# Optimization experiments

Measured on AMD Instinct MI355X. Metric: run time of the kernel, lower is better.

The kernel has to match this reference:

```python
import jax, jax.numpy as jnp
import numpy as np

H = 128
N_CAN = 100000
N_FLAG = 50000
E = 600000
L = 500000


def _sage_conv(x_src, x_dst, edge_index, Wl, bl, Wr):
    # PyG SAGEConv (mean aggr): lin_l(mean_{j in N(i)} x_j) + lin_r(x_i)
    src, dst = edge_index[0], edge_index[1]
    msg = x_src[src]                                        # [E, H] gather
    n_dst = x_dst.shape[0]
    agg = jax.ops.segment_sum(msg, dst, num_segments=n_dst)  # [N_dst, H]
    cnt = jax.ops.segment_sum(jnp.ones((msg.shape[0],), msg.dtype), dst,
                              num_segments=n_dst)
    mean = agg / jnp.maximum(cnt, 1.0)[:, None]
    return mean @ Wl.T + bl + x_dst @ Wr.T


def setup_inputs() -> dict:
    key = jax.random.key(0)
    ks = jax.random.split(key, 16)
    s = 1.0 / np.sqrt(H)
    inp = {
        'can_node_id': jnp.arange(N_CAN, dtype=jnp.int64) if jax.config.jax_enable_x64 else jnp.arange(N_CAN, dtype=jnp.int32),
        'flag_node_id': jnp.arange(N_FLAG, dtype=jnp.int32),
        'edge_index_cf': jnp.stack([
            jax.random.randint(ks[0], (E,), 0, N_CAN),
            jax.random.randint(ks[1], (E,), 0, N_FLAG)]),
        'edge_index_fc': jnp.stack([
            jax.random.randint(ks[2], (E,), 0, N_FLAG),
            jax.random.randint(ks[3], (E,), 0, N_CAN)]),
        'edge_label_index': jnp.stack([
            jax.random.randint(ks[4], (L,), 0, N_CAN),
            jax.random.randint(ks[5], (L,), 0, N_FLAG)]),
        'can_emb': jax.random.normal(ks[6], (N_CAN, H), jnp.float32),
        'flag_emb': jax.random.normal(ks[7], (N_FLAG, H), jnp.float32),
        # SAGEConv for edge type CAN->flag (updates flag nodes)
        'Wl_cf': jax.random.normal(ks[8], (H, H), jnp.float32) * s,
        'bl_cf': jnp.zeros((H,), jnp.float32),
        'Wr_cf': jax.random.normal(ks[9], (H, H), jnp.float32) * s,
        # SAGEConv for edge type flag->CAN (updates CAN nodes)
        'Wl_fc': jax.random.normal(ks[10], (H, H), jnp.float32) * s,
        'bl_fc': jnp.zeros((H,), jnp.float32),
        'Wr_fc': jax.random.normal(ks[11], (H, H), jnp.float32) * s,
        # classifier MLP
        'W1': jax.random.normal(ks[12], (H, 2 * H), jnp.float32) * (1.0 / np.sqrt(2 * H)),
        'b1': jnp.zeros((H,), jnp.float32),
        'W2': jax.random.normal(ks[13], (1, H), jnp.float32) * s,
        'b2': jnp.zeros((1,), jnp.float32),
    }
    return inp


def reference(can_node_id, flag_node_id, edge_index_cf, edge_index_fc,
              edge_label_index, can_emb, flag_emb,
              Wl_cf, bl_cf, Wr_cf, Wl_fc, bl_fc, Wr_fc,
              W1, b1, W2, b2):
    # embedding lookups
    x_can = can_emb[can_node_id]    # [N_CAN, H]
    x_flag = flag_emb[flag_node_id]  # [N_FLAG, H]
    # to_hetero single SAGE layer + relu (dropout is identity in eval)
    upd_flag = jax.nn.relu(_sage_conv(x_can, x_flag, edge_index_cf, Wl_cf, bl_cf, Wr_cf))
    upd_can = jax.nn.relu(_sage_conv(x_flag, x_can, edge_index_fc, Wl_fc, bl_fc, Wr_fc))
    # link prediction classifier
    src = upd_can[edge_label_index[0]]   # [L, H]
    dst = upd_flag[edge_label_index[1]]  # [L, H]
    h = jax.nn.relu(jnp.concatenate([src, dst], axis=-1) @ W1.T + b1)
    out = h @ W2.T + b2
    return out.reshape(-1)
```

## Files before the change

### kernel.cpp

```cpp
#include <hip/hip_runtime.h>
#include <hip/hip_bf16.h>

#define H 128
#define BSH 8
#define MAXB 1024

typedef __attribute__((ext_vector_type(8))) short short8;
typedef __attribute__((ext_vector_type(4))) short short4v;
typedef __attribute__((ext_vector_type(4))) float floatx4;
typedef unsigned short ushort_t;
typedef unsigned int uint_t;

__device__ __forceinline__ short f2bf(float f) {
    __hip_bfloat16 h = __float2bfloat16(f);
    return *reinterpret_cast<short*>(&h);
}
__device__ __forceinline__ float bflo(uint_t u) { return __uint_as_float(u << 16); }
__device__ __forceinline__ float bfhi(uint_t u) { return __uint_as_float(u & 0xFFFF0000u); }
__device__ __forceinline__ uint_t pack_bf2(float x, float y) {
    return (uint_t)(ushort_t)f2bf(x) | ((uint_t)(ushort_t)f2bf(y) << 16);
}

__global__ __launch_bounds__(256)
void bucket_hist_cvt_kernel(const int* __restrict__ ei1, const int* __restrict__ ei2,
                            int E, int NF, int B, int* __restrict__ bcnt, int nbh,
                            const float* __restrict__ a, int n4a,
                            const float* __restrict__ b, int n4b,
                            ushort_t* __restrict__ da, ushort_t* __restrict__ db,
                            const float* __restrict__ Wl_cf, const float* __restrict__ Wr_cf,
                            const float* __restrict__ Wl_fc, const float* __restrict__ Wr_fc,
                            const float* __restrict__ W1, ushort_t* __restrict__ wb) {
    __shared__ int h[MAXB];
    int tid = threadIdx.x;
    if ((int)blockIdx.x < nbh) {
        for (int i = tid; i < B; i += 256) h[i] = 0;
        __syncthreads();
        int base = blockIdx.x * 4096;
        #pragma unroll 4
        for (int it = 0; it < 16; ++it) {
            int t = base + it * 256 + tid;
            if (t < 2 * E) {
                int g = (t < E) ? ei1[E + t] : (ei2[E + t - E] + NF);
                atomicAdd(&h[g >> BSH], 1);
            }
        }
        __syncthreads();
        for (int i = tid; i < B; i += 256)
            if (h[i]) atomicAdd(&bcnt[i], h[i]);
        return;
    }
    int i = ((int)blockIdx.x - nbh) * 256 + tid;
    const float* src; ushort_t* dst; int k;
    if (i < n4a) { src = a; dst = da; k = i; }
    else if (i < n4a + n4b) { src = b; dst = db; k = i - n4a; }
    else {
        int idx = (i - n4a - n4b) * 4;
        if (idx >= 98304) return;
        int off;
        if      (idx < 16384) { src = Wl_cf; off = idx; }
        else if (idx < 32768) { src = Wr_cf; off = idx - 16384; }
        else if (idx < 49152) { src = Wl_fc; off = idx - 32768; }
        else if (idx < 65536) { src = Wr_fc; off = idx - 49152; }
        else                  { src = W1;    off = idx - 65536; }
        float4 v = *(const float4*)(src + off);
        short4v s;
        s[0] = f2bf(v.x); s[1] = f2bf(v.y); s[2] = f2bf(v.z); s[3] = f2bf(v.w);
        *(short4v*)(wb + idx) = s;
        return;
    }
    float4 v = ((const float4*)src)[k];
    short4v s;
    s[0] = f2bf(v.x); s[1] = f2bf(v.y); s[2] = f2bf(v.z); s[3] = f2bf(v.w);
    ((short4v*)dst)[k] = s;
}

__global__ __launch_bounds__(256)
void partition_kernel(const int* __restrict__ ei1, const int* __restrict__ ei2,
                      int E, int NF, int B, const int* __restrict__ bcnt,
                      int* __restrict__ bfront, uint_t* __restrict__ part) {
    __shared__ int h[MAXB];
    __shared__ int basex[MAXB];
    __shared__ int sdata[256];
    int tid = threadIdx.x;
    {
        int base4 = tid * 4;
        int v[4]; int s = 0;
        #pragma unroll
        for (int i = 0; i < 4; ++i) { int idx = base4 + i; v[i] = (idx < B) ? bcnt[idx] : 0; s += v[i]; }
        sdata[tid] = s;
        __syncthreads();
        for (int off = 1; off < 256; off <<= 1) {
            int t = (tid >= off) ? sdata[tid - off] : 0;
            __syncthreads();
            sdata[tid] += t;
            __syncthreads();
        }
        int excl = tid ? sdata[tid - 1] : 0;
        #pragma unroll
        for (int i = 0; i < 4; ++i) {
            int idx = base4 + i;
            if (idx < B) basex[idx] = excl;
            excl += v[i];
        }
    }
    for (int i = tid; i < B; i += 256) h[i] = 0;
    __syncthreads();
    int base = blockIdx.x * 4096;
    #pragma unroll 4
    for (int it = 0; it < 16; ++it) {
        int t = base + it * 256 + tid;
        if (t < 2 * E) {
            int g = (t < E) ? ei1[E + t] : (ei2[E + t - E] + NF);
            atomicAdd(&h[g >> BSH], 1);
        }
    }
    __syncthreads();
    for (int i = tid; i < B; i += 256) {
        int c = h[i];
        if (c) basex[i] += atomicAdd(&bfront[i], c);
    }
    __syncthreads();
    for (int i = tid; i < B; i += 256) h[i] = 0;
    __syncthreads();
    #pragma unroll 4
    for (int it = 0; it < 16; ++it) {
        int t = base + it * 256 + tid;
        if (t < 2 * E) {
            int g, s;
            if (t < E) { g = ei1[E + t]; s = ei1[t]; }
            else       { int e = t - E; g = ei2[E + e] + NF; s = ei2[e]; }
            int bk = g >> BSH;
            int r = atomicAdd(&h[bk], 1);
            part[basex[bk] + r] = ((uint_t)(g & 255) << 24) | (uint_t)s;
        }
    }
}

__global__ __launch_bounds__(256)
void fine_bin_kernel(const int* __restrict__ bcnt, int B, int nTot, int E2,
                     const uint_t* __restrict__ part,
                     int* __restrict__ offs, int* __restrict__ bins) {
    __shared__ int cnt[256];
    __shared__ int sdata[256];
    __shared__ int excl[256];
    int b = blockIdx.x;
    int tid = threadIdx.x;
    {
        int partial = 0;
        for (int i = tid; i < b; i += 256) partial += bcnt[i];
        sdata[tid] = partial;
        __syncthreads();
        for (int off = 128; off > 0; off >>= 1) {
            if (tid < off) sdata[tid] += sdata[tid + off];
            __syncthreads();
        }
    }
    int seg0 = sdata[0];
    int seg1 = seg0 + bcnt[b];
    int gbase = b << BSH;
    __syncthreads();
    cnt[tid] = 0;
    __syncthreads();
    for (int k = seg0 + tid; k < seg1; k += 256)
        atomicAdd(&cnt[part[k] >> 24], 1);
    __syncthreads();
    sdata[tid] = cnt[tid];
    __syncthreads();
    for (int off = 1; off < 256; off <<= 1) {
        int t = (tid >= off) ? sdata[tid - off] : 0;
        __syncthreads();
        sdata[tid] += t;
        __syncthreads();
    }
    excl[tid] = tid ? sdata[tid - 1] : 0;
    int g = gbase + tid;
    if (g < nTot) offs[g] = seg0 + excl[tid];
    if (b == 0 && tid == 0) offs[nTot] = E2;
    cnt[tid] = 0;
    __syncthreads();
    for (int k = seg0 + tid; k < seg1; k += 256) {
        uint_t e = part[k];
        int l = (int)(e >> 24);
        int r = atomicAdd(&cnt[l], 1);
        bins[seg0 + excl[l] + r] = (int)(e & 0x00FFFFFFu);
    }
}

__global__ __launch_bounds__(256)
void gather_mean3_kernel(const int* __restrict__ offs, int nTotal, int split,
                         const int* __restrict__ bins,
                         const ushort_t* __restrict__ embA, ushort_t* __restrict__ aggA,
                         const ushort_t* __restrict__ embB, ushort_t* __restrict__ aggB) {
    int g = blockIdx.x * 4 + (threadIdx.x >> 6);
    if (g >= nTotal) return;
    int lane = threadIdx.x & 63;
    int q = lane >> 4, l15 = lane & 15;
    int start = offs[g];
    int end = offs[g + 1];
    int deg = end - start;
    const ushort_t* emb; ushort_t* agg; int row;
    if (g < split) { emb = embA; agg = aggA; row = g; }
    else           { emb = embB; agg = aggB; row = g - split; }

    float acc[8];
    #pragma unroll
    for (int t = 0; t < 8; ++t) acc[t] = 0.f;

    int nPre = deg < 64 ? deg : 64;
    int pre = (lane < nPre) ? bins[start + lane] : 0;

    int col = l15 * 8;
    for (int it = 0; it < (nPre + 7) / 8; ++it) {
        int e0 = 8 * it + q;
        int e1 = e0 + 4;
        int s0 = __shfl(pre, e0, 64);
        int s1 = __shfl(pre, e1, 64);
        if (e0 < nPre) {
            uint4 r = *(const uint4*)(emb + (size_t)s0 * H + col);
            acc[0] += bflo(r.x); acc[1] += bfhi(r.x);
            acc[2] += bflo(r.y); acc[3] += bfhi(r.y);
            acc[4] += bflo(r.z); acc[5] += bfhi(r.z);
            acc[6] += bflo(r.w); acc[7] += bfhi(r.w);
        }
        if (e1 < nPre) {
            uint4 r = *(const uint4*)(emb + (size_t)s1 * H + col);
            acc[0] += bflo(r.x); acc[1] += bfhi(r.x);
            acc[2] += bflo(r.y); acc[3] += bfhi(r.y);
            acc[4] += bflo(r.z); acc[5] += bfhi(r.z);
            acc[6] += bflo(r.w); acc[7] += bfhi(r.w);
        }
    }
    for (int k = start + 64 + q; k < end; k += 4) {
        int s = bins[k];
        uint4 r = *(const uint4*)(emb + (size_t)s * H + col);
        acc[0] += bflo(r.x); acc[1] += bfhi(r.x);
        acc[2] += bflo(r.y); acc[3] += bfhi(r.y);
        acc[4] += bflo(r.z); acc[5] += bfhi(r.z);
        acc[6] += bflo(r.w); acc[7] += bfhi(r.w);
    }

    #pragma unroll
    for (int t = 0; t < 8; ++t) {
        acc[t] += __shfl_xor(acc[t], 16, 64);
        acc[t] += __shfl_xor(acc[t], 32, 64);
    }
    if (q == 0) {
        float inv = 1.0f / fmaxf((float)deg, 1.0f);
        uint4 o;
        o.x = pack_bf2(acc[0] * inv, acc[1] * inv);
        o.y = pack_bf2(acc[2] * inv, acc[3] * inv);
        o.z = pack_bf2(acc[4] * inv, acc[5] * inv);
        o.w = pack_bf2(acc[6] * inv, acc[7] * inv);
        *(uint4*)(agg + (size_t)row * H + col) = o;
    }
}

__global__ __launch_bounds__(256)
void sage2_kernel(int nbF, int NF, int NC,
                  ushort_t* __restrict__ aggf, const ushort_t* __restrict__ embf,
                  ushort_t* __restrict__ aggc, const ushort_t* __restrict__ embc,
                  const ushort_t* __restrict__ wlf, const ushort_t* __restrict__ wrf,
                  const float* __restrict__ blf,
                  const ushort_t* __restrict__ wlc, const ushort_t* __restrict__ wrc,
                  const float* __restrict__ blc,
                  const ushort_t* __restrict__ W1) {
    __shared__ short A[64][264];
    bool isF = (int)blockIdx.x < nbF;
    int nrows = isF ? NF : NC;
    int rbase = (isF ? blockIdx.x : blockIdx.x - nbF) * 64;
    ushort_t* io = isF ? aggf : aggc;
    const ushort_t* emb = isF ? embf : embc;
    const ushort_t* Wl = isF ? wlf : wlc;
    const ushort_t* Wr = isF ? wrf : wrc;
    const float* bl = isF ? blf : blc;
    int koff = isF ? 128 : 0;

    int tid = threadIdx.x;
    int lane = tid & 63;
    int wv = tid >> 6;
    int l15 = lane & 15;
    int quad = lane >> 4;
    int nb0 = 32 * wv + l15;

    for (int idx = tid; idx < 64 * 64; idx += 256) {
        int r = idx >> 6, qq = idx & 63;
        int row = rbase + r;
        short4v s = (short4v){0, 0, 0, 0};
        if (row < nrows) {
            const ushort_t* src = (qq < 32) ? (io + (size_t)row * H + qq * 4)
                                            : (emb + (size_t)row * H + (qq - 32) * 4);
            s = *(const short4v*)src;
        }
        *(short4v*)&A[r][qq * 4] = s;
    }

    floatx4 acc[4][2];
    #pragma unroll
    for (int i = 0; i < 4; ++i)
        #pragma unroll
        for (int j = 0; j < 2; ++j)
            acc[i][j] = (floatx4){0.f, 0.f, 0.f, 0.f};

    float blv0 = bl[nb0];
    float blv1 = bl[nb0 + 16];
    __syncthreads();

    #pragma unroll
    for (int half = 0; half < 2; ++half) {
        const ushort_t* W = half ? Wr : Wl;
        #pragma unroll
        for (int ks = 0; ks < 4; ++ks) {
            int kb = ks * 32 + quad * 8;
            short8 b0 = *(const short8*)(W + (size_t)nb0 * H + kb);
            short8 b1 = *(const short8*)(W + (size_t)(nb0 + 16) * H + kb);
            int ka = half * 128 + kb;
            #pragma unroll
            for (int mt = 0; mt < 4; ++mt) {
                short8 a = *(const short8*)&A[16 * mt + l15][ka];
                acc[mt][0] = __builtin_amdgcn_mfma_f32_16x16x32_bf16(a, b0, acc[mt][0], 0, 0, 0);
                acc[mt][1] = __builtin_amdgcn_mfma_f32_16x16x32_bf16(a, b1, acc[mt][1], 0, 0, 0);
            }
        }
    }

    __syncthreads();
    #pragma unroll
    for (int mt = 0; mt < 4; ++mt)
        #pragma unroll
        for (int nt = 0; nt < 2; ++nt) {
            float blv = nt ? blv1 : blv0;
            int colw = nb0 + 16 * nt;
            #pragma unroll
            for (int rg = 0; rg < 4; ++rg) {
                int row = 16 * mt + quad * 4 + rg;
                A[row][colw] = f2bf(fmaxf(acc[mt][nt][rg] + blv, 0.0f));
                acc[mt][nt][rg] = 0.0f;
            }
        }
    __syncthreads();

    const ushort_t* W1p = W1 + koff;
    #pragma unroll
    for (int ks = 0; ks < 4; ++ks) {
        int kb = ks * 32 + quad * 8;
        short8 b0 = *(const short8*)(W1p + (size_t)nb0 * 256 + kb);
        short8 b1 = *(const short8*)(W1p + (size_t)(nb0 + 16) * 256 + kb);
        #pragma unroll
        for (int mt = 0; mt < 4; ++mt) {
            short8 a = *(const short8*)&A[16 * mt + l15][kb];
            acc[mt][0] = __builtin_amdgcn_mfma_f32_16x16x32_bf16(a, b0, acc[mt][0], 0, 0, 0);
            acc[mt][1] = __builtin_amdgcn_mfma_f32_16x16x32_bf16(a, b1, acc[mt][1], 0, 0, 0);
        }
    }

    #pragma unroll
    for (int mt = 0; mt < 4; ++mt)
        #pragma unroll
        for (int rg = 0; rg < 4; ++rg) {
            int row = rbase + 16 * mt + quad * 4 + rg;
            if (row < nrows) {
                io[(size_t)row * H + nb0]      = (ushort_t)f2bf(acc[mt][0][rg]);
                io[(size_t)row * H + nb0 + 16] = (ushort_t)f2bf(acc[mt][1][rg]);
            }
        }
}

__global__ __launch_bounds__(256)
void hist2_kernel(const int* __restrict__ ei1, const int* __restrict__ ei2, int E,
                  int* __restrict__ deg1, int* __restrict__ deg2) {
    int t = blockIdx.x * 256 + threadIdx.x;
    if (t < E) atomicAdd(&deg1[ei1[E + t]], 1);
    else if (t < 2 * E) { int e = t - E; atomicAdd(&deg2[ei2[E + e]], 1); }
}

__global__ __launch_bounds__(256)
void scan_blocksum_kernel(const int* __restrict__ deg, int n, int* __restrict__ bsums) {
    __shared__ int sdata[256];
    int tid = threadIdx.x;
    int base = blockIdx.x * 1024 + tid * 4;
    int v = 0;
    #pragma unroll
    for (int i = 0; i < 4; ++i) { int idx = base + i; if (idx < n) v += deg[idx]; }
    sdata[tid] = v;
    __syncthreads();
    for (int off = 128; off > 0; off >>= 1) {
        if (tid < off) sdata[tid] += sdata[tid + off];
        __syncthreads();
    }
    if (tid == 0) bsums[blockIdx.x] = sdata[0];
}

__global__ __launch_bounds__(256)
void scan_write_kernel(int* __restrict__ data, int n, const int* __restrict__ bsums) {
    __shared__ int sdata[256];
    __shared__ int boff;
    int tid = threadIdx.x;
    if (tid < 64) {
        int acc = 0;
        for (int i = tid; i < (int)blockIdx.x; i += 64) acc += bsums[i];
        #pragma unroll
        for (int off = 32; off > 0; off >>= 1) acc += __shfl_xor(acc, off, 64);
        if (tid == 0) boff = acc;
    }
    int base = blockIdx.x * 1024 + tid * 4;
    int v[4]; int s = 0;
    #pragma unroll
    for (int i = 0; i < 4; ++i) { int idx = base + i; v[i] = (idx < n) ? data[idx] : 0; s += v[i]; }
    sdata[tid] = s;
    __syncthreads();
    for (int off = 1; off < 256; off <<= 1) {
        int t = (tid >= off) ? sdata[tid - off] : 0;
        __syncthreads();
        sdata[tid] += t;
        __syncthreads();
    }
    int excl = (tid == 0 ? 0 : sdata[tid - 1]) + boff;
    #pragma unroll
    for (int i = 0; i < 4; ++i) {
        int idx = base + i;
        if (idx < n) data[idx] = excl;
        excl += v[i];
    }
}

__global__ __launch_bounds__(256)
void incl_to_start_kernel(const int* __restrict__ incl, int nTot, int* __restrict__ offs) {
    int g = blockIdx.x * 256 + threadIdx.x;
    if (g < nTot) offs[g + 1] = incl[g];
    if (g == 0) offs[0] = 0;
}

__global__ __launch_bounds__(256)
void bin2_kernel(const int* __restrict__ ei1, const int* __restrict__ ei2, int E,
                 int* __restrict__ offs1, int* __restrict__ offs2,
                 int* __restrict__ bins) {
    int t = blockIdx.x * 256 + threadIdx.x;
    if (t < E) {
        int pos = atomicAdd(&offs1[ei1[E + t]], 1);
        bins[pos] = ei1[t];
    } else if (t < 2 * E) {
        int e = t - E;
        int pos = atomicAdd(&offs2[ei2[E + e]], 1);
        bins[pos] = ei2[e];
    }
}

__global__ __launch_bounds__(256)
void classify_kernel(const int* __restrict__ eli, int L,
                     const ushort_t* __restrict__ u_can,
                     const ushort_t* __restrict__ u_flag,
                     const float* __restrict__ b1,
                     const float* __restrict__ W2,
                     const float* __restrict__ b2,
                     float* __restrict__ out) {
    int tid = threadIdx.x;
    int lane = tid & 63;
    int wv = tid >> 6;
    int sub = lane >> 4;
    int l15 = lane & 15;
    int p = blockIdx.x * 16 + wv * 4 + sub;
    if (p >= L) return;
    int i = eli[p];
    int j = eli[L + p];
    uint4 a = ((const uint4*)(u_can  + (size_t)i * H))[l15];
    uint4 b = ((const uint4*)(u_flag + (size_t)j * H))[l15];
    float4 bb0 = ((const float4*)b1)[l15 * 2];
    float4 bb1 = ((const float4*)b1)[l15 * 2 + 1];
    float4 w0  = ((const float4*)W2)[l15 * 2];
    float4 w1  = ((const float4*)W2)[l15 * 2 + 1];
    float s = fmaxf(bflo(a.x) + bflo(b.x) + bb0.x, 0.f) * w0.x
            + fmaxf(bfhi(a.x) + bfhi(b.x) + bb0.y, 0.f) * w0.y
            + fmaxf(bflo(a.y) + bflo(b.y) + bb0.z, 0.f) * w0.z
            + fmaxf(bfhi(a.y) + bfhi(b.y) + bb0.w, 0.f) * w0.w
            + fmaxf(bflo(a.z) + bflo(b.z) + bb1.x, 0.f) * w1.x
            + fmaxf(bfhi(a.z) + bfhi(b.z) + bb1.y, 0.f) * w1.y
            + fmaxf(bflo(a.w) + bflo(b.w) + bb1.z, 0.f) * w1.z
            + fmaxf(bfhi(a.w) + bfhi(b.w) + bb1.w, 0.f) * w1.w;
    #pragma unroll
    for (int off = 8; off > 0; off >>= 1)
        s += __shfl_down(s, off, 16);
    if (l15 == 0) out[p] = s + b2[0];
}

extern "C" void kernel_launch(void* const* d_in, const int* in_sizes, int n_in,
                              void* d_out, int out_size, void* d_ws, size_t ws_size,
                              hipStream_t stream) {
    const int*   ei_cf    = (const int*)d_in[2];
    const int*   ei_fc    = (const int*)d_in[3];
    const int*   eli      = (const int*)d_in[4];
    const float* can_emb  = (const float*)d_in[5];
    const float* flag_emb = (const float*)d_in[6];
    const float* Wl_cf    = (const float*)d_in[7];
    const float* bl_cf    = (const float*)d_in[8];
    const float* Wr_cf    = (const float*)d_in[9];
    const float* Wl_fc    = (const float*)d_in[10];
    const float* bl_fc    = (const float*)d_in[11];
    const float* Wr_fc    = (const float*)d_in[12];
    const float* W1       = (const float*)d_in[13];
    const float* b1       = (const float*)d_in[14];
    const float* W2       = (const float*)d_in[15];
    const float* b2       = (const float*)d_in[16];
    float* out = (float*)d_out;

    const int NCAN  = in_sizes[0];
    const int NFLAG = in_sizes[1];
    const int E     = in_sizes[2] / 2;
    const int L     = in_sizes[4] / 2;
    const int nTot  = NCAN + NFLAG;
    const int B     = (nTot + 255) >> BSH;

    ushort_t* aggc = (ushort_t*)d_ws;
    ushort_t* aggf = aggc + (size_t)NCAN * H;
    ushort_t* embc = aggf + (size_t)NFLAG * H;
    ushort_t* embf = embc + (size_t)NCAN * H;
    char* tail = (char*)(embf + (size_t)NFLAG * H);
    size_t tail_off = (size_t)(tail - (char*)d_ws);

    int nbF = (NFLAG + 63) / 64, nbC = (NCAN + 63) / 64;
    int n4c = NCAN * H / 4, n4f = NFLAG * H / 4;
    int nbcvt = (n4c + n4f + 24576 + 255) / 256;

    size_t off_offs  = tail_off;
    size_t off_bcnt  = off_offs  + (size_t)(nTot + 1) * 4;
    size_t off_bfrnt = off_bcnt  + (size_t)MAXB * 4;
    size_t off_bins  = off_bfrnt + (size_t)MAXB * 4;
    size_t off_part  = off_bins  + (size_t)2 * E * 4;
    size_t off_wb    = off_part  + (size_t)2 * E * 4;
    size_t need_new  = off_wb + 98304 * 2;

    int* offs   = (int*)((char*)d_ws + off_offs);
    int* bcnt   = (int*)((char*)d_ws + off_bcnt);
    int* bfront = (int*)((char*)d_ws + off_bfrnt);
    int* bins   = (int*)((char*)d_ws + off_bins);

    if (ws_size >= need_new && B <= MAXB) {
        uint_t* part = (uint_t*)((char*)d_ws + off_part);
        ushort_t* wb = (ushort_t*)((char*)d_ws + off_wb);
        ushort_t* wb_wlcf = wb, *wb_wrcf = wb + 16384, *wb_wlfc = wb + 32768,
                 *wb_wrfc = wb + 49152, *wb_w1 = wb + 65536;

        int nbh = (2 * E + 4095) >> 12;
        hipMemsetAsync(bcnt, 0, (size_t)2 * MAXB * 4, stream);
        bucket_hist_cvt_kernel<<<nbh + nbcvt, 256, 0, stream>>>(
            ei_cf, ei_fc, E, NFLAG, B, bcnt, nbh,
            can_emb, n4c, flag_emb, n4f, embc, embf,
            Wl_cf, Wr_cf, Wl_fc, Wr_fc, W1, wb);
        partition_kernel<<<nbh, 256, 0, stream>>>(ei_cf, ei_fc, E, NFLAG, B, bcnt, bfront, part);
        fine_bin_kernel<<<B, 256, 0, stream>>>(bcnt, B, nTot, 2 * E, part, offs, bins);
        gather_mean3_kernel<<<(nTot + 3) / 4, 256, 0, stream>>>(
            offs, nTot, NFLAG, bins, embc, aggf, embf, aggc);
        sage2_kernel<<<nbF + nbC, 256, 0, stream>>>(
            nbF, NFLAG, NCAN, aggf, embf, aggc, embc,
            wb_wlcf, wb_wrcf, bl_cf, wb_wlfc, wb_wrfc, bl_fc, wb_w1);
    } else {
        int* scanf_ = bins;
        int* scanc_ = scanf_ + NFLAG;
        int* bins2  = scanc_ + NCAN;
        int* bsums  = bins2 + 2 * E;
        ushort_t* wb = (ushort_t*)(bsums + 256);
        ushort_t* wb_wlcf = wb, *wb_wrcf = wb + 16384, *wb_wlfc = wb + 32768,
                 *wb_wrfc = wb + 49152, *wb_w1 = wb + 65536;

        bucket_hist_cvt_kernel<<<nbcvt, 256, 0, stream>>>(
            ei_cf, ei_fc, E, NFLAG, B, bcnt, 0,
            can_emb, n4c, flag_emb, n4f, embc, embf,
            Wl_cf, Wr_cf, Wl_fc, Wr_fc, W1, wb);
        hipMemsetAsync(scanf_, 0, ((size_t)NFLAG + NCAN) * 4, stream);
        int nb = (nTot + 1023) / 1024;
        hist2_kernel<<<(2 * E + 255) / 256, 256, 0, stream>>>(ei_cf, ei_fc, E, scanf_, scanc_);
        scan_blocksum_kernel<<<nb, 256, 0, stream>>>(scanf_, nTot, bsums);
        scan_write_kernel<<<nb, 256, 0, stream>>>(scanf_, nTot, bsums);
        bin2_kernel<<<(2 * E + 255) / 256, 256, 0, stream>>>(ei_cf, ei_fc, E, scanf_, scanc_, bins2);
        incl_to_start_kernel<<<(nTot + 255) / 256, 256, 0, stream>>>(scanf_, nTot, offs);
        gather_mean3_kernel<<<(nTot + 3) / 4, 256, 0, stream>>>(
            offs, nTot, NFLAG, bins2, embc, aggf, embf, aggc);
        sage2_kernel<<<nbF + nbC, 256, 0, stream>>>(
            nbF, NFLAG, NCAN, aggf, embf, aggc, embc,
            wb_wlcf, wb_wrcf, bl_cf, wb_wlfc, wb_wrfc, bl_fc, wb_w1);
    }

    classify_kernel<<<(L + 15) / 16, 256, 0, stream>>>(
        eli, L, aggc, aggf, b1, W2, b2, out);
}
```

Before: 339.8 us.

## Fuse neighbor mean gather into SAGE GEMM kernel via shared memory

Removes the separate gather_mean3 kernel and computes each 64-row tile's neighbor means directly into the shared-memory A tile inside the SAGE matmul kernel. This avoids writing the bf16 aggregate rows to global memory and reading them back, and saves one launch. In exchange, each block's gather now runs with only 4 waves doing 16 rows each, sequentially before the MFMA phase. That lowers memory-level parallelism for the irregular gathers and may hurt latency hiding.

Measured after the change: 352.7 us. 1.04x slower.

```diff
diff --git a/kernel.cpp b/kernel.cpp
--- a/kernel.cpp
+++ b/kernel.cpp
@@ -187,93 +187,27 @@
 }
 
 __global__ __launch_bounds__(256)
-void gather_mean3_kernel(const int* __restrict__ offs, int nTotal, int split,
-                         const int* __restrict__ bins,
-                         const ushort_t* __restrict__ embA, ushort_t* __restrict__ aggA,
-                         const ushort_t* __restrict__ embB, ushort_t* __restrict__ aggB) {
-    int g = blockIdx.x * 4 + (threadIdx.x >> 6);
-    if (g >= nTotal) return;
-    int lane = threadIdx.x & 63;
-    int q = lane >> 4, l15 = lane & 15;
-    int start = offs[g];
-    int end = offs[g + 1];
-    int deg = end - start;
-    const ushort_t* emb; ushort_t* agg; int row;
-    if (g < split) { emb = embA; agg = aggA; row = g; }
-    else           { emb = embB; agg = aggB; row = g - split; }
-
-    float acc[8];
-    #pragma unroll
-    for (int t = 0; t < 8; ++t) acc[t] = 0.f;
-
-    int nPre = deg < 64 ? deg : 64;
-    int pre = (lane < nPre) ? bins[start + lane] : 0;
-
-    int col = l15 * 8;
-    for (int it = 0; it < (nPre + 7) / 8; ++it) {
-        int e0 = 8 * it + q;
-        int e1 = e0 + 4;
-        int s0 = __shfl(pre, e0, 64);
-        int s1 = __shfl(pre, e1, 64);
-        if (e0 < nPre) {
-            uint4 r = *(const uint4*)(emb + (size_t)s0 * H + col);
-            acc[0] += bflo(r.x); acc[1] += bfhi(r.x);
-            acc[2] += bflo(r.y); acc[3] += bfhi(r.y);
-            acc[4] += bflo(r.z); acc[5] += bfhi(r.z);
-            acc[6] += bflo(r.w); acc[7] += bfhi(r.w);
-        }
-        if (e1 < nPre) {
-            uint4 r = *(const uint4*)(emb + (size_t)s1 * H + col);
-            acc[0] += bflo(r.x); acc[1] += bfhi(r.x);
-            acc[2] += bflo(r.y); acc[3] += bfhi(r.y);
-            acc[4] += bflo(r.z); acc[5] += bfhi(r.z);
-            acc[6] += bflo(r.w); acc[7] += bfhi(r.w);
-        }
-    }
-    for (int k = start + 64 + q; k < end; k += 4) {
-        int s = bins[k];
-        uint4 r = *(const uint4*)(emb + (size_t)s * H + col);
-        acc[0] += bflo(r.x); acc[1] += bfhi(r.x);
-        acc[2] += bflo(r.y); acc[3] += bfhi(r.y);
-        acc[4] += bflo(r.z); acc[5] += bfhi(r.z);
-        acc[6] += bflo(r.w); acc[7] += bfhi(r.w);
-    }
-
-    #pragma unroll
-    for (int t = 0; t < 8; ++t) {
-        acc[t] += __shfl_xor(acc[t], 16, 64);
-        acc[t] += __shfl_xor(acc[t], 32, 64);
-    }
-    if (q == 0) {
-        float inv = 1.0f / fmaxf((float)deg, 1.0f);
-        uint4 o;
-        o.x = pack_bf2(acc[0] * inv, acc[1] * inv);
-        o.y = pack_bf2(acc[2] * inv, acc[3] * inv);
-        o.z = pack_bf2(acc[4] * inv, acc[5] * inv);
-        o.w = pack_bf2(acc[6] * inv, acc[7] * inv);
-        *(uint4*)(agg + (size_t)row * H + col) = o;
-    }
-}
-
-__global__ __launch_bounds__(256)
-void sage2_kernel(int nbF, int NF, int NC,
-                  ushort_t* __restrict__ aggf, const ushort_t* __restrict__ embf,
-                  ushort_t* __restrict__ aggc, const ushort_t* __restrict__ embc,
-                  const ushort_t* __restrict__ wlf, const ushort_t* __restrict__ wrf,
-                  const float* __restrict__ blf,
-                  const ushort_t* __restrict__ wlc, const ushort_t* __restrict__ wrc,
-                  const float* __restrict__ blc,
-                  const ushort_t* __restrict__ W1) {
+void sage2g_kernel(int nbF, int NF, int NC,
+                   const int* __restrict__ offs, const int* __restrict__ bins,
+                   ushort_t* __restrict__ outf, const ushort_t* __restrict__ embf,
+                   ushort_t* __restrict__ outc, const ushort_t* __restrict__ embc,
+                   const ushort_t* __restrict__ wlf, const ushort_t* __restrict__ wrf,
+                   const float* __restrict__ blf,
+                   const ushort_t* __restrict__ wlc, const ushort_t* __restrict__ wrc,
+                   const float* __restrict__ blc,
+                   const ushort_t* __restrict__ W1) {
     __shared__ short A[64][264];
     bool isF = (int)blockIdx.x < nbF;
     int nrows = isF ? NF : NC;
     int rbase = (isF ? blockIdx.x : blockIdx.x - nbF) * 64;
-    ushort_t* io = isF ? aggf : aggc;
-    const ushort_t* emb = isF ? embf : embc;
+    ushort_t* io = isF ? outf : outc;
+    const ushort_t* embS = isF ? embf : embc;
+    const ushort_t* embN = isF ? embc : embf;
     const ushort_t* Wl = isF ? wlf : wlc;
     const ushort_t* Wr = isF ? wrf : wrc;
     const float* bl = isF ? blf : blc;
     int koff = isF ? 128 : 0;
+    int gofs = isF ? 0 : NF;
 
     int tid = threadIdx.x;
     int lane = tid & 63;
@@ -282,16 +216,74 @@
     int quad = lane >> 4;
     int nb0 = 32 * wv + l15;
 
-    for (int idx = tid; idx < 64 * 64; idx += 256) {
-        int r = idx >> 6, qq = idx & 63;
+    for (int idx = tid; idx < 64 * 32; idx += 256) {
+        int r = idx >> 5, c = idx & 31;
         int row = rbase + r;
         short4v s = (short4v){0, 0, 0, 0};
-        if (row < nrows) {
-            const ushort_t* src = (qq < 32) ? (io + (size_t)row * H + qq * 4)
-                                            : (emb + (size_t)row * H + (qq - 32) * 4);
-            s = *(const short4v*)src;
-        }
-        *(short4v*)&A[r][qq * 4] = s;
+        if (row < nrows) s = *(const short4v*)(embS + (size_t)row * H + c * 4);
+        *(short4v*)&A[r][128 + c * 4] = s;
+    }
+
+    {
+        int col = l15 * 8;
+        for (int i = 0; i < 16; ++i) {
+            int r = wv * 16 + i;
+            int row = rbase + r;
+            int start = 0, end = 0;
+            if (row < nrows) { int g = gofs + row; start = offs[g]; end = offs[g + 1]; }
+            int deg = end - start;
+
+            float acc[8];
+            #pragma unroll
+            for (int t = 0; t < 8; ++t) acc[t] = 0.f;
+
+            int nPre = deg < 64 ? deg : 64;
+            int pre = (lane < nPre) ? bins[start + lane] : 0;
+
+            for (int it = 0; it < (nPre + 7) / 8; ++it) {
+                int e0 = 8 * it + quad;
+                int e1 = e0 + 4;
+                int s0 = __shfl(pre, e0, 64);
+                int s1 = __shfl(pre, e1, 64);
+                if (e0 < nPre) {
+                    uint4 rr = *(const uint4*)(embN + (size_t)s0 * H + col);
+                    acc[0] += bflo(rr.x); acc[1] += bfhi(rr.x);
+                    acc[2] += bflo(rr.y); acc[3] += bfhi(rr.y);
+                    acc[4] += bflo(rr.z); acc[5] += bfhi(rr.z);
+                    acc[6] += bflo(rr.w); acc[7] += bfhi(rr.w);
+                }
+                if (e1 < nPre) {
+                    uint4 rr = *(const uint4*)(embN + (size_t)s1 * H + col);
+                    acc[0] += bflo(rr.x); acc[1] += bfhi(rr.x);
+                    acc[2] += bflo(rr.y); acc[3] += bfhi(rr.y);
+                    acc[4] += bflo(rr.z); acc[5] += bfhi(rr.z);
+                    acc[6] += bflo(rr.w); acc[7] += bfhi(rr.w);
+                }
+            }
+            for (int k = start + 64 + quad; k < end; k += 4) {
+                int s = bins[k];
+                uint4 rr = *(const uint4*)(embN + (size_t)s * H + col);
+                acc[0] += bflo(rr.x); acc[1] += bfhi(rr.x);
+                acc[2] += bflo(rr.y); acc[3] += bfhi(rr.y);
+                acc[4] += bflo(rr.z); acc[5] += bfhi(rr.z);
+                acc[6] += bflo(rr.w); acc[7] += bfhi(rr.w);
+            }
+
+            #pragma unroll
+            for (int t = 0; t < 8; ++t) {
+                acc[t] += __shfl_xor(acc[t], 16, 64);
+                acc[t] += __shfl_xor(acc[t], 32, 64);
+            }
+            if (quad == 0) {
+                float inv = 1.0f / fmaxf((float)deg, 1.0f);
+                uint4 o;
+                o.x = pack_bf2(acc[0] * inv, acc[1] * inv);
+                o.y = pack_bf2(acc[2] * inv, acc[3] * inv);
+                o.z = pack_bf2(acc[4] * inv, acc[5] * inv);
+                o.w = pack_bf2(acc[6] * inv, acc[7] * inv);
+                *(uint4*)&A[r][col] = o;
+            }
+        }
     }
 
     floatx4 acc[4][2];
@@ -547,10 +539,9 @@
             Wl_cf, Wr_cf, Wl_fc, Wr_fc, W1, wb);
         partition_kernel<<<nbh, 256, 0, stream>>>(ei_cf, ei_fc, E, NFLAG, B, bcnt, bfront, part);
         fine_bin_kernel<<<B, 256, 0, stream>>>(bcnt, B, nTot, 2 * E, part, offs, bins);
-        gather_mean3_kernel<<<(nTot + 3) / 4, 256, 0, stream>>>(
-            offs, nTot, NFLAG, bins, embc, aggf, embf, aggc);
-        sage2_kernel<<<nbF + nbC, 256, 0, stream>>>(
-            nbF, NFLAG, NCAN, aggf, embf, aggc, embc,
+        sage2g_kernel<<<nbF + nbC, 256, 0, stream>>>(
+            nbF, NFLAG, NCAN, offs, bins,
+            aggf, embf, aggc, embc,
             wb_wlcf, wb_wrcf, bl_cf, wb_wlfc, wb_wrfc, bl_fc, wb_w1);
     } else {
         int* scanf_ = bins;
@@ -572,10 +563,9 @@
         scan_write_kernel<<<nb, 256, 0, stream>>>(scanf_, nTot, bsums);
         bin2_kernel<<<(2 * E + 255) / 256, 256, 0, stream>>>(ei_cf, ei_fc, E, scanf_, scanc_, bins2);
         incl_to_start_kernel<<<(nTot + 255) / 256, 256, 0, stream>>>(scanf_, nTot, offs);
-        gather_mean3_kernel<<<(nTot + 3) / 4, 256, 0, stream>>>(
-            offs, nTot, NFLAG, bins2, embc, aggf, embf, aggc);
-        sage2_kernel<<<nbF + nbC, 256, 0, stream>>>(
-            nbF, NFLAG, NCAN, aggf, embf, aggc, embc,
+        sage2g_kernel<<<nbF + nbC, 256, 0, stream>>>(
+            nbF, NFLAG, NCAN, offs, bins2,
+            aggf, embf, aggc, embc,
             wb_wlcf, wb_wrcf, bl_cf, wb_wlfc, wb_wrfc, bl_fc, wb_w1);
     }
 
```
